# Kernel tuning notes

Measured on AMD Instinct MI355X. Metric: run time of the kernel, lower is better.

## Reference

```python
import jax, jax.numpy as jnp
import numpy as np

D_MODEL = 128; D_STATE = 16; D_CONV = 4; EXPAND = 2
D_INNER = EXPAND * D_MODEL          # 256
DT_RANK = (D_MODEL + 15) // 16      # 8 (ceil(d_model/16), Mamba default)
B, NF, H, W = 4, 32, 16, 16         # L = NF*H*W = 8192 tokens


def _layer_norm(x, w, b, eps=1e-5):
    m = x.mean(-1, keepdims=True)
    v = ((x - m) ** 2).mean(-1, keepdims=True)
    return (x - m) * jax.lax.rsqrt(v + eps) * w + b


def _causal_conv(x, w, b):
    # x: [B, L, D_INNER]; w: [D_INNER, 1, D_CONV] depthwise causal conv along L
    y = jax.lax.conv_general_dilated(
        jnp.swapaxes(x, 1, 2), w, (1,), [(D_CONV - 1, 0)],
        dimension_numbers=('NCH', 'OIH', 'NCH'), feature_group_count=D_INNER)
    return jnp.swapaxes(y + b[None, :, None], 1, 2)


def _mamba_dir(xi, z, conv_w, conv_b, xproj_w, dtproj_w, dtproj_b, A_log, Dskip):
    # One direction of the bidirectional Mamba block (selective scan).
    xc = jax.nn.silu(_causal_conv(xi, conv_w, conv_b))            # [B,L,Di]
    dbl = xc @ xproj_w.T                                          # [B,L,dt_rank+2n]
    dt_r, Bm, Cm = jnp.split(dbl, [DT_RANK, DT_RANK + D_STATE], axis=-1)
    dt = jax.nn.softplus(dt_r @ dtproj_w.T + dtproj_b)            # [B,L,Di]
    A = -jnp.exp(A_log)                                           # [Di,n]

    def step(h, inp):
        dt_t, B_t, C_t, x_t = inp                                 # [B,Di],[B,n],[B,n],[B,Di]
        h = jnp.exp(dt_t[:, :, None] * A) * h + (dt_t * x_t)[:, :, None] * B_t[:, None, :]
        return h, jnp.einsum('bdn,bn->bd', h, C_t)

    h0 = jnp.zeros((xi.shape[0], D_INNER, D_STATE), xi.dtype)
    xs = tuple(jnp.swapaxes(a, 0, 1) for a in (dt, Bm, Cm, xc))   # L-leading
    _, ys = jax.lax.scan(step, h0, xs)                            # [L,B,Di]
    y = jnp.swapaxes(ys, 0, 1) + xc * Dskip
    return y * jax.nn.silu(z)


def setup_inputs() -> dict:
    key = jax.random.key(0)
    ks = jax.random.split(key, 12)
    wrand = lambda k, shape: jax.random.normal(k, shape, jnp.float32) * 0.02
    # S4D-real init: A = [1..d_state] per channel
    A_init = jnp.log(jnp.tile(jnp.arange(1, D_STATE + 1, dtype=jnp.float32)[None, :], (D_INNER, 1)))
    dt_bias = jnp.full((D_INNER,), -4.6, jnp.float32)  # softplus^-1(~0.01)
    return {
        'x': jax.random.normal(ks[0], (B, D_MODEL, NF, H, W), jnp.float32),
        'ln1_w': jnp.ones((D_MODEL,), jnp.float32), 'ln1_b': jnp.zeros((D_MODEL,), jnp.float32),
        'ln2_w': jnp.ones((D_MODEL,), jnp.float32), 'ln2_b': jnp.zeros((D_MODEL,), jnp.float32),
        'in_proj_w': wrand(ks[1], (2 * D_INNER, D_MODEL)),
        'out_proj_w': wrand(ks[2], (D_MODEL, D_INNER)),
        'conv_w_f': wrand(ks[3], (D_INNER, 1, D_CONV)), 'conv_b_f': jnp.zeros((D_INNER,), jnp.float32),
        'xproj_w_f': wrand(ks[4], (DT_RANK + 2 * D_STATE, D_INNER)),
        'dtproj_w_f': wrand(ks[5], (D_INNER, DT_RANK)), 'dtproj_b_f': dt_bias,
        'A_log_f': A_init, 'D_f': jnp.ones((D_INNER,), jnp.float32),
        'conv_w_b': wrand(ks[6], (D_INNER, 1, D_CONV)), 'conv_b_b': jnp.zeros((D_INNER,), jnp.float32),
        'xproj_w_b': wrand(ks[7], (DT_RANK + 2 * D_STATE, D_INNER)),
        'dtproj_w_b': wrand(ks[8], (D_INNER, DT_RANK)), 'dtproj_b_b': dt_bias,
        'A_log_b': A_init, 'D_b': jnp.ones((D_INNER,), jnp.float32),
    }


def reference(x, ln1_w, ln1_b, ln2_w, ln2_b, in_proj_w, out_proj_w,
              conv_w_f, conv_b_f, xproj_w_f, dtproj_w_f, dtproj_b_f, A_log_f, D_f,
              conv_w_b, conv_b_b, xproj_w_b, dtproj_w_b, dtproj_b_b, A_log_b, D_b):
    b, d, nf, h, w = x.shape
    L = nf * h * w
    x_flat = jnp.swapaxes(x.reshape(b, d, L), 1, 2)               # [B,L,d_model]
    xn = _layer_norm(x_flat, ln1_w, ln1_b)
    xz = xn @ in_proj_w.T                                          # [B,L,2*Di]
    xi, z = jnp.split(xz, 2, axis=-1)
    y_f = _mamba_dir(xi, z, conv_w_f, conv_b_f, xproj_w_f, dtproj_w_f, dtproj_b_f, A_log_f, D_f)
    y_b = _mamba_dir(xi[:, ::-1], z[:, ::-1], conv_w_b, conv_b_b, xproj_w_b,
                     dtproj_w_b, dtproj_b_b, A_log_b, D_b)[:, ::-1]
    out = (y_f + y_b) @ out_proj_w.T                               # shared out_proj
    x_out = _layer_norm(x_flat + out, ln2_w, ln2_b)                # residual + norm2
    return jnp.swapaxes(x_out, 1, 2).reshape(b, d, nf, h, w)
```

## Files before the change

### kernel.cpp

```cpp
#include <hip/hip_runtime.h>

#define NB   4
#define LSEQ 8192
#define DM   128
#define DI   256
#define NS   16
#define RK   8
#define NCH  256
#define LC   32
#define MTOT (NB*LSEQ)
#define LOG2E 1.44269504088896340736f
#define LN2f  0.69314718055994530942f

#if __has_builtin(__builtin_amdgcn_exp2f)
__device__ __forceinline__ float fexp2(float x){ return __builtin_amdgcn_exp2f(x); }
#else
__device__ __forceinline__ float fexp2(float x){ return exp2f(x); }
#endif
#if __has_builtin(__builtin_amdgcn_logf)
__device__ __forceinline__ float flog2(float x){ return __builtin_amdgcn_logf(x); }
#else
__device__ __forceinline__ float flog2(float x){ return log2f(x); }
#endif
#if __has_builtin(__builtin_amdgcn_rcpf)
__device__ __forceinline__ float frcp(float x){ return __builtin_amdgcn_rcpf(x); }
#else
__device__ __forceinline__ float frcp(float x){ return 1.f/x; }
#endif
__device__ __forceinline__ float fexpn(float x){ return fexp2(x*LOG2E); }
__device__ __forceinline__ float fsilu(float x){ return x*frcp(1.f + fexpn(-x)); }
__device__ __forceinline__ float fsoftplus(float x){
  return fmaxf(x,0.f) + flog2(1.f + fexpn(-fabsf(x)))*LN2f;
}

__device__ __forceinline__ unsigned short f2bf(float v){
  unsigned int u = __float_as_uint(v);
  return (unsigned short)((u + 0x7FFFu + ((u >> 16) & 1u)) >> 16);
}
__device__ __forceinline__ float bf2f(unsigned short h){
  return __uint_as_float(((unsigned int)h) << 16);
}

typedef __attribute__((ext_vector_type(8))) short bf16x8;
typedef __attribute__((ext_vector_type(4))) float f32x4;
typedef __attribute__((ext_vector_type(2))) float f32x2;

#if __has_builtin(__builtin_elementwise_fma)
__device__ __forceinline__ f32x2 pkfma(f32x2 a, f32x2 b, f32x2 c){ return __builtin_elementwise_fma(a,b,c); }
#else
__device__ __forceinline__ f32x2 pkfma(f32x2 a, f32x2 b, f32x2 c){ return a*b + c; }
#endif

__global__ __launch_bounds__(256) void k_prep_w(
    const float* __restrict__ wip, unsigned short* __restrict__ wipbf,
    const float* __restrict__ xwf, const float* __restrict__ xwb, unsigned short* __restrict__ xwbf,
    const float* __restrict__ wop, unsigned short* __restrict__ wopbf)
{
  int i = blockIdx.x*256 + threadIdx.x;
  if (i < 65536) {
    wipbf[i] = f2bf(wip[i]);
  } else if (i < 90112) {
    int j = i - 65536;
    int dirw = j / 12288;
    int rem = j - dirw*12288;
    int row = rem >> 8, k = rem & 255;
    const float* src = dirw ? xwb : xwf;
    xwbf[j] = (row < 40) ? f2bf(src[row*256 + k]) : (unsigned short)0;
  } else {
    int j = i - 90112;
    wopbf[j] = f2bf(wop[j]);
  }
}

__global__ __launch_bounds__(256) void k_ln(
    const float* __restrict__ x, const float* __restrict__ ln1w, const float* __restrict__ ln1b,
    unsigned short* __restrict__ xnbf)
{
  __shared__ float a_s[DM][65];
  __shared__ float mS[64], rS[64];
  const int tid = threadIdx.x;
  const int m0 = blockIdx.x * 64;
  const int b = m0 >> 13, l0 = m0 & (LSEQ-1);
  const float* xb = x + b*DM*LSEQ;
#pragma unroll
  for (int i = 0; i < 32; ++i) {
    int idx = tid + i*256;
    int d = idx >> 6, l = idx & 63;
    a_s[d][l] = xb[d*LSEQ + l0 + l];
  }
  __syncthreads();
  {
    int p = tid & 3, l = tid >> 2;
    float s = 0.f, q = 0.f;
#pragma unroll
    for (int jj = 0; jj < 32; ++jj) {
      float v = a_s[p + 4*jj][l];
      s += v; q += v*v;
    }
    s += __shfl_xor(s,1); s += __shfl_xor(s,2);
    q += __shfl_xor(q,1); q += __shfl_xor(q,2);
    float m = s*(1.f/DM);
    float var = q*(1.f/DM) - m*m;
    if (p == 0) { mS[l] = m; rS[l] = rsqrtf(var + 1e-5f); }
  }
  __syncthreads();
#pragma unroll
  for (int i = 0; i < 32; ++i) {
    int idx = tid + i*256;
    int l = idx >> 7, d = idx & 127;
    float v = (a_s[d][l] - mS[l])*rS[l]*ln1w[d] + ln1b[d];
    xnbf[(m0+l)*DM + d] = f2bf(v);
  }
}

__global__ __launch_bounds__(256) void k_gemm_in(
    const unsigned short* __restrict__ xnbf, const unsigned short* __restrict__ wipbf,
    unsigned short* __restrict__ xib, unsigned short* __restrict__ zzb)
{
  __shared__ char lds[32768];
  const int tid = threadIdx.x;
  const int m0 = blockIdx.x * 64;
  const int n0 = blockIdx.y * 64;
  const unsigned short* srcs[2] = { xnbf + m0*DM, wipbf + n0*DM };
#pragma unroll
  for (int p = 0; p < 2; ++p) {
#pragma unroll
    for (int i = 0; i < 4; ++i) {
      int u = tid + i*256;
      int row = u >> 4, c = u & 15;
      int dstu = p*1024 + row*16 + (c ^ (row & 7));
      *(uint4*)(lds + dstu*16) = *(const uint4*)(srcs[p] + row*DM + c*8);
    }
  }
  __syncthreads();
  const int wid = tid >> 6, lane = tid & 63;
  const int m0w = (wid & 1)*32, n0w = (wid >> 1)*32;
  const int lr = lane & 15, kg = lane >> 4;
  bf16x8 af[2][4], bfv[2][4];
#pragma unroll
  for (int mi = 0; mi < 2; ++mi) {
    int row = m0w + mi*16 + lr;
#pragma unroll
    for (int kk = 0; kk < 4; ++kk) {
      int slot = (kk*4 + kg) ^ (row & 7);
      af[mi][kk] = *(const bf16x8*)(lds + row*256 + slot*16);
    }
  }
#pragma unroll
  for (int nj = 0; nj < 2; ++nj) {
    int row = n0w + nj*16 + lr;
#pragma unroll
    for (int kk = 0; kk < 4; ++kk) {
      int slot = (kk*4 + kg) ^ (row & 7);
      bfv[nj][kk] = *(const bf16x8*)(lds + 16384 + row*256 + slot*16);
    }
  }
  f32x4 acc[2][2];
#pragma unroll
  for (int mi = 0; mi < 2; ++mi)
#pragma unroll
    for (int nj = 0; nj < 2; ++nj) acc[mi][nj] = 0.f;
#pragma unroll
  for (int kk = 0; kk < 4; ++kk)
#pragma unroll
    for (int mi = 0; mi < 2; ++mi)
#pragma unroll
      for (int nj = 0; nj < 2; ++nj)
        acc[mi][nj] = __builtin_amdgcn_mfma_f32_16x16x32_bf16(af[mi][kk], bfv[nj][kk], acc[mi][nj], 0,0,0);
  if (n0 < 256) {
#pragma unroll
    for (int mi = 0; mi < 2; ++mi)
#pragma unroll
      for (int nj = 0; nj < 2; ++nj) {
        int n_g = n0 + n0w + nj*16 + lr;
#pragma unroll
        for (int r = 0; r < 4; ++r) {
          int m_g = m0 + m0w + mi*16 + kg*4 + r;
          xib[(size_t)m_g*DI + n_g] = f2bf(acc[mi][nj][r]);
        }
      }
  } else {
#pragma unroll
    for (int mi = 0; mi < 2; ++mi)
#pragma unroll
      for (int nj = 0; nj < 2; ++nj) {
        int n_g = (n0 - 256) + n0w + nj*16 + lr;
#pragma unroll
        for (int r = 0; r < 4; ++r) {
          int m_g = m0 + m0w + mi*16 + kg*4 + r;
          zzb[(size_t)m_g*DI + n_g] = f2bf(fsilu(acc[mi][nj][r]));
        }
      }
  }
}

__global__ __launch_bounds__(256) void k_conv_xproj(
  const unsigned short* __restrict__ xib,
  const float* __restrict__ cwf, const float* __restrict__ cbf,
  const float* __restrict__ cwb, const float* __restrict__ cbb,
  const unsigned short* __restrict__ xwbf,
  const float* __restrict__ dtwf, const float* __restrict__ dtbf,
  const float* __restrict__ dtwb, const float* __restrict__ dtbb,
  float* __restrict__ BC,
  uint4* __restrict__ xdt4)
{
  __shared__ char lds[57344];
  __shared__ float dtr_s[64][8];
  const int tid = threadIdx.x, bid = blockIdx.x;
  const int lt = bid & (LSEQ/64 - 1);
  const int b  = (bid >> 7) & 3;
  const int dir = bid >> 9;
  const int l0 = lt*64;
  const int db = dir*NB + b;
  const unsigned short* xwp = xwbf + dir*48*256;
#pragma unroll
  for (int i = 0; i < 6; ++i) {
    int u = tid + i*256;
    int row = u >> 5, s = u & 31;
    *(uint4*)(lds + 32768 + row*512 + ((s ^ (row & 7))<<4)) =
        *(const uint4*)(xwp + row*256 + s*8);
  }
  const float* cw  = dir ? cwb : cwf;
  const float* cbp = dir ? cbb : cbf;
  const int d = tid;
  const float w0 = cw[d*4+0], w1 = cw[d*4+1], w2 = cw[d*4+2], w3 = cw[d*4+3];
  const float bias = cbp[d];
  const int g0 = dir ? (LSEQ-1-l0) : l0;
  const int stp = dir ? -DI : DI;
  const unsigned short* xp = xib + (size_t)(b*LSEQ)*DI + d + (size_t)g0*DI;
  float h3 = 0.f, h2 = 0.f, h1 = 0.f;
  if (l0 >= 3) { h3 = bf2f(xp[-3*stp]); h2 = bf2f(xp[-2*stp]); h1 = bf2f(xp[-1*stp]); }
  float r0 = bf2f(xp[0]), r1 = bf2f(xp[stp]), r2 = bf2f(xp[2*stp]), r3 = bf2f(xp[3*stp]);
  for (int j = 0; j < 64; j += 4) {
    float v0 = r0, v1 = r1, v2 = r2, v3 = r3;
    if (j + 4 < 64) {
      const unsigned short* q = xp + (j+4)*stp;
      r0 = bf2f(q[0]); r1 = bf2f(q[stp]); r2 = bf2f(q[2*stp]); r3 = bf2f(q[3*stp]);
    }
#pragma unroll
    for (int u = 0; u < 4; ++u) {
      float vv = (u==0)?v0:(u==1)?v1:(u==2)?v2:v3;
      float a = bias + w0*h3 + w1*h2 + w2*h1 + w3*vv;
      int row = j + u;
      *(unsigned short*)(lds + row*512 + ((((d>>3) ^ (row&7))<<4) + ((d&7)<<1))) = f2bf(fsilu(a));
      h3 = h2; h2 = h1; h1 = vv;
    }
  }
  __syncthreads();
  const int wid = tid >> 6, lane = tid & 63;
  const int lr = lane & 15, kg = lane >> 4;
  const int arow = wid*16 + lr;
  f32x4 acc[3];
#pragma unroll
  for (int j = 0; j < 3; ++j) acc[j] = 0.f;
#pragma unroll
  for (int t = 0; t < 8; ++t) {
    bf16x8 afv = *(const bf16x8*)(lds + arow*512 + (((t*4+kg) ^ (arow&7))<<4));
#pragma unroll
    for (int j = 0; j < 3; ++j) {
      int wrow = j*16 + lr;
      bf16x8 bfr = *(const bf16x8*)(lds + 32768 + wrow*512 + (((t*4+kg) ^ (wrow&7))<<4));
      acc[j] = __builtin_amdgcn_mfma_f32_16x16x32_bf16(afv, bfr, acc[j], 0,0,0);
    }
  }
  const int base_l = (db*LSEQ + l0) + wid*16 + kg*4;
  const int rloc = wid*16 + kg*4;
#pragma unroll
  for (int j = 0; j < 3; ++j) {
    int col = j*16 + lr;
#pragma unroll
    for (int r = 0; r < 4; ++r) {
      float v = acc[j][r];
      if (col < 8)       dtr_s[rloc + r][col] = v;
      else if (col < 40) BC[(size_t)(base_l + r)*32 + (col - 8)] = v;
    }
  }
  __syncthreads();
  const float* dtw = dir ? dtwb : dtwf;
  const float* dtbp= dir ? dtbb : dtbf;
  float dwv[8];
  *(float4*)(dwv+0) = *(const float4*)&dtw[d*RK];
  *(float4*)(dwv+4) = *(const float4*)&dtw[d*RK+4];
  const float dtbv = dtbp[d];
  uint4* xdtp = xdt4 + (size_t)(db*(LSEQ/4) + (l0>>2))*DI + d;
  unsigned int a4[4];
  for (int row = 0; row < 64; ++row) {
    float sd = dtbv;
#pragma unroll
    for (int r = 0; r < RK; ++r) sd = fmaf(dtr_s[row][r], dwv[r], sd);
    unsigned short dtb = f2bf(fsoftplus(sd));
    unsigned short xcb = *(const unsigned short*)(lds + row*512 + ((((d>>3) ^ (row&7))<<4) + ((d&7)<<1)));
    a4[row & 3] = (unsigned int)xcb | ((unsigned int)dtb << 16);
    if ((row & 3) == 3)
      xdtp[(size_t)(row >> 2)*DI] = make_uint4(a4[0], a4[1], a4[2], a4[3]);
  }
}

__global__ __launch_bounds__(256) void k_scan_local(
  const uint4* __restrict__ xdt4, const float* __restrict__ BC,
  const float* __restrict__ alogf, const float* __restrict__ alogb,
  unsigned short* __restrict__ hloc, float* __restrict__ sumdt)
{
  const int tid = threadIdx.x, bid = blockIdx.x;
  const int c = bid & (NCH-1), b = (bid>>8)&3, dir = bid>>10;
  const int db = dir*NB + b;
  const int l0 = c*LC;
  const float* alog = dir ? alogb : alogf;
  const int d = tid;
  float A2[NS];
#pragma unroll
  for (int n = 0; n < NS; ++n) A2[n] = -fexpn(alog[d*NS+n]) * LOG2E;
  const float a20 = A2[0];
  bool pw = true;
#pragma unroll
  for (int n = 1; n < NS; ++n) pw = pw && (fabsf(A2[n] - (n+1)*a20) <= 1e-3f*fabsf(A2[n]));
  f32x2 h2[8];
#pragma unroll
  for (int k = 0; k < 8; ++k) h2[k] = 0.f;
  const uint4* xq = xdt4 + (size_t)(db*(LSEQ/4) + (l0>>2))*DI + d;
  const float* BCb = BC + (size_t)(db*LSEQ + l0)*32;
  uint4 X0 = xq[0];
  uint4 X1 = xq[DI];
  float sac = 0.f;
  for (int g = 0; g < 8; ++g) {
    uint4 cur = X0;
    X0 = X1;
    if (g + 2 < 8) X1 = xq[(size_t)(g+2)*DI];
    unsigned int us[4] = {cur.x, cur.y, cur.z, cur.w};
#pragma unroll
    for (int u = 0; u < 4; ++u) {
      unsigned int uu = us[u];
      float xc = __uint_as_float(uu << 16);
      float dt = __uint_as_float(uu & 0xffff0000u);
      sac += dt;
      float dx = dt*xc;
      const float4* bq = (const float4*)(BCb + (size_t)(g*4+u)*32);
      float bcl[16];
      *(float4*)(bcl+0)  = bq[0];
      *(float4*)(bcl+4)  = bq[1];
      *(float4*)(bcl+8)  = bq[2];
      *(float4*)(bcl+12) = bq[3];
      const f32x2* bb2 = (const f32x2*)bcl;
      f32x2 e2[8];
      if (pw) {
        float e1 = fexp2(a20*dt);
        float es = e1*e1;
        f32x2 esq = {es, es};
        e2[0] = (f32x2){e1, es};
#pragma unroll
        for (int k = 1; k < 8; ++k) e2[k] = e2[k-1]*esq;
      } else {
#pragma unroll
        for (int k = 0; k < 8; ++k)
          e2[k] = (f32x2){fexp2(A2[2*k]*dt), fexp2(A2[2*k+1]*dt)};
      }
      f32x2 dx2 = {dx, dx};
#pragma unroll
      for (int k = 0; k < 8; ++k) h2[k] = pkfma(h2[k], e2[k], bb2[k]*dx2);
    }
  }
  unsigned int hp8[8];
#pragma unroll
  for (int k = 0; k < 8; ++k)
    hp8[k] = (unsigned int)f2bf(h2[k].x) | ((unsigned int)f2bf(h2[k].y) << 16);
  unsigned short* dst = hloc + ((size_t)(db*NCH + c)*DI + d)*NS;
  *(uint4*)(dst)   = *(uint4*)(hp8);
  *(uint4*)(dst+8) = *(uint4*)(hp8+4);
  sumdt[(size_t)(db*NCH + c)*DI + d] = sac;
}

__global__ __launch_bounds__(64) void k_prefix(
  unsigned short* __restrict__ hloc, const float* __restrict__ sumdt,
  const float* __restrict__ alogf, const float* __restrict__ alogb)
{
  const int gid = blockIdx.x*64 + threadIdx.x;
  const int n = gid & 15;
  const int d = (gid >> 4) & 255;
  const int db = gid >> 12;
  const float* alog = (db >= NB) ? alogb : alogf;
  const float a2 = -fexpn(alog[d*NS+n]) * LOG2E;
  const int HS = DI*NS;
  unsigned short* hp = hloc + (size_t)db*NCH*HS + d*NS + n;
  const float* sp = sumdt + (size_t)db*NCH*DI + d;
  float hr = 0.f;
  float bl[16], bs[16];
#pragma unroll
  for (int j = 0; j < 16; ++j) { bl[j] = bf2f(hp[(size_t)j*HS]); bs[j] = sp[(size_t)j*DI]; }
  for (int blk = 0; blk < NCH/16; ++blk) {
    float nl[16], nsv[16];
    if (blk < NCH/16 - 1) {
#pragma unroll
      for (int j = 0; j < 16; ++j) {
        nl[j]  = bf2f(hp[(size_t)(blk*16+16+j)*HS]);
        nsv[j] = sp[(size_t)(blk*16+16+j)*DI];
      }
    }
#pragma unroll
    for (int j = 0; j < 16; ++j) {
      float hl = bl[j];
      hp[(size_t)(blk*16+j)*HS] = f2bf(hr);
      hr = fmaf(fexp2(a2*bs[j]), hr, hl);
    }
    if (blk < NCH/16 - 1) {
#pragma unroll
      for (int j = 0; j < 16; ++j) { bl[j] = nl[j]; bs[j] = nsv[j]; }
    }
  }
}

__global__ __launch_bounds__(256) void k_scan_out(
  const uint4* __restrict__ xdt4, const unsigned short* __restrict__ zzb,
  const float* __restrict__ BC,
  const unsigned short* __restrict__ hinb,
  const float* __restrict__ alogf, const float* __restrict__ alogb,
  const float* __restrict__ Dskf, const float* __restrict__ Dskb,
  unsigned short* __restrict__ s2bf)
{
  const int tid = threadIdx.x, bid = blockIdx.x;
  const int c = bid & (NCH-1), b = (bid>>8)&3, dir = bid>>10;
  const int db = dir*NB + b;
  const int l0 = c*LC;
  const float* alog = dir ? alogb : alogf;
  const int d = tid;
  const float Dd = (dir ? Dskb : Dskf)[d];
  float A2[NS];
#pragma unroll
  for (int n = 0; n < NS; ++n) A2[n] = -fexpn(alog[d*NS+n]) * LOG2E;
  const float a20 = A2[0];
  bool pw = true;
#pragma unroll
  for (int n = 1; n < NS; ++n) pw = pw && (fabsf(A2[n] - (n+1)*a20) <= 1e-3f*fabsf(A2[n]));
  f32x2 h2[8];
  {
    const unsigned short* hb = hinb + ((size_t)(db*NCH + c)*DI + d)*NS;
    uint4 p0 = *(const uint4*)(hb);
    uint4 p1 = *(const uint4*)(hb+8);
    unsigned int w[8] = {p0.x,p0.y,p0.z,p0.w,p1.x,p1.y,p1.z,p1.w};
#pragma unroll
    for (int k = 0; k < 8; ++k)
      h2[k] = (f32x2){__uint_as_float(w[k] << 16), __uint_as_float(w[k] & 0xffff0000u)};
  }
  const int g0 = dir ? (LSEQ-1-l0) : l0;
  const int stp = dir ? -DI : DI;
  const uint4* xq = xdt4 + (size_t)(db*(LSEQ/4) + (l0>>2))*DI + d;
  const float* BCb = BC + (size_t)(db*LSEQ + l0)*32;
  const unsigned short* zp = zzb + (size_t)(b*LSEQ + g0)*DI + d;
  unsigned short* sp = s2bf + (size_t)(db*LSEQ + l0)*DI + d;
  uint4 X0 = xq[0];
  uint4 X1 = xq[DI];
  unsigned short zA[4], zB[4];
#pragma unroll
  for (int k = 0; k < 4; ++k) { zA[k] = zp[k*stp]; zB[k] = zp[(4+k)*stp]; }
  for (int g = 0; g < 8; ++g) {
    uint4 cur = X0;
    X0 = X1;
    if (g + 2 < 8) X1 = xq[(size_t)(g+2)*DI];
    unsigned short zc[4];
#pragma unroll
    for (int k = 0; k < 4; ++k) zc[k] = zA[k];
#pragma unroll
    for (int k = 0; k < 4; ++k) zA[k] = zB[k];
    if (g + 2 < 8) {
#pragma unroll
      for (int k = 0; k < 4; ++k) zB[k] = zp[((g+2)*4+k)*stp];
    }
    unsigned int us[4] = {cur.x, cur.y, cur.z, cur.w};
#pragma unroll
    for (int u = 0; u < 4; ++u) {
      unsigned int uu = us[u];
      float xc = __uint_as_float(uu << 16);
      float dt = __uint_as_float(uu & 0xffff0000u);
      float dx = dt*xc;
      const float4* bq = (const float4*)(BCb + (size_t)(g*4+u)*32);
      float bcl[32];
      *(float4*)(bcl+0)  = bq[0];
      *(float4*)(bcl+4)  = bq[1];
      *(float4*)(bcl+8)  = bq[2];
      *(float4*)(bcl+12) = bq[3];
      *(float4*)(bcl+16) = bq[4];
      *(float4*)(bcl+20) = bq[5];
      *(float4*)(bcl+24) = bq[6];
      *(float4*)(bcl+28) = bq[7];
      const f32x2* bb2 = (const f32x2*)bcl;
      const f32x2* cc2 = (const f32x2*)(bcl + 16);
      f32x2 e2[8];
      if (pw) {
        float e1 = fexp2(a20*dt);
        float es = e1*e1;
        f32x2 esq = {es, es};
        e2[0] = (f32x2){e1, es};
#pragma unroll
        for (int k = 1; k < 8; ++k) e2[k] = e2[k-1]*esq;
      } else {
#pragma unroll
        for (int k = 0; k < 8; ++k)
          e2[k] = (f32x2){fexp2(A2[2*k]*dt), fexp2(A2[2*k+1]*dt)};
      }
      f32x2 dx2 = {dx, dx};
      f32x2 yv2 = {0.f, 0.f};
#pragma unroll
      for (int k = 0; k < 8; ++k) {
        h2[k] = pkfma(h2[k], e2[k], bb2[k]*dx2);
        yv2 = pkfma(h2[k], cc2[k], yv2);
      }
      float yv = yv2.x + yv2.y;
      yv = fmaf(xc, Dd, yv);
      sp[(size_t)(g*4+u)*DI] = f2bf(yv * bf2f(zc[u]));
    }
  }
}

__global__ __launch_bounds__(512) void k_out(
  const unsigned short* __restrict__ s2bf,
  const unsigned short* __restrict__ wopbf,
  const float* __restrict__ x, const float* __restrict__ ln2w, const float* __restrict__ ln2b,
  float* __restrict__ out)
{
  __shared__ char lds[65536];
  const int tid = threadIdx.x;
  const int m0 = blockIdx.x*64;
  const int b = m0 >> 13, l0 = m0 & (LSEQ-1);
  const unsigned short* sF = s2bf + (size_t)b*LSEQ*DI;
  const unsigned short* sB = s2bf + (size_t)(NB + b)*LSEQ*DI;
#pragma unroll
  for (int i = 0; i < 8; ++i) {
    int u = tid + i*512;
    int row = u >> 6, c = u & 63;
    int l = l0 + row;
    const unsigned short* src = (c < 32) ? (sF + (size_t)l*DI + c*8)
                                         : (sB + (size_t)(LSEQ-1-l)*DI + (c-32)*8);
    *(uint4*)(lds + row*1024 + ((c ^ (row & 7))<<4)) = *(const uint4*)src;
  }
  const int wid = tid >> 6;
  const int wr = wid >> 2, wc = wid & 3;
  const int lane = tid & 63, lr = lane & 15, kg = lane >> 4;
  bf16x8 wf[2][8];
#pragma unroll
  for (int nt = 0; nt < 2; ++nt) {
    int n = wc*32 + nt*16 + lr;
#pragma unroll
    for (int kt = 0; kt < 8; ++kt)
      wf[nt][kt] = *(const bf16x8*)(wopbf + n*DI + kt*32 + kg*8);
  }
  __syncthreads();
  f32x4 acc[2][2];
#pragma unroll
  for (int mt = 0; mt < 2; ++mt)
#pragma unroll
    for (int nt = 0; nt < 2; ++nt) acc[mt][nt] = 0.f;
#pragma unroll
  for (int kt2 = 0; kt2 < 16; ++kt2) {
#pragma unroll
    for (int mt = 0; mt < 2; ++mt) {
      int row = wr*32 + mt*16 + lr;
      int slot = (kt2*4 + kg) ^ (row & 7);
      bf16x8 af = *(const bf16x8*)(lds + row*1024 + (slot<<4));
#pragma unroll
      for (int nt = 0; nt < 2; ++nt)
        acc[mt][nt] = __builtin_amdgcn_mfma_f32_16x16x32_bf16(af, wf[nt][kt2 & 7], acc[mt][nt], 0,0,0);
    }
  }
  __syncthreads();
  float* smem = (float*)lds;
  const int RP = 133;
  float* mS = smem + 64*RP;
  float* rS = mS + 64;
  const float* xb = x + b*DM*LSEQ + l0;
#pragma unroll
  for (int mt = 0; mt < 2; ++mt) {
    int mbase = wr*32 + mt*16 + kg*4;
#pragma unroll
    for (int nt = 0; nt < 2; ++nt) {
      int n = wc*32 + nt*16 + lr;
      float4 rx = *(const float4*)&xb[n*LSEQ + mbase];
      smem[(mbase+0)*RP + n] = acc[mt][nt][0] + rx.x;
      smem[(mbase+1)*RP + n] = acc[mt][nt][1] + rx.y;
      smem[(mbase+2)*RP + n] = acc[mt][nt][2] + rx.z;
      smem[(mbase+3)*RP + n] = acc[mt][nt][3] + rx.w;
    }
  }
  __syncthreads();
  {
    int row = tid >> 3, p = tid & 7;
    float s = 0.f, q = 0.f;
#pragma unroll
    for (int jj = 0; jj < 16; ++jj) {
      float v = smem[row*RP + p*16 + jj];
      s += v; q += v*v;
    }
    s += __shfl_xor(s,1); s += __shfl_xor(s,2); s += __shfl_xor(s,4);
    q += __shfl_xor(q,1); q += __shfl_xor(q,2); q += __shfl_xor(q,4);
    if (p == 0) {
      float m = s*(1.f/DM);
      float var = q*(1.f/DM) - m*m;
      mS[row] = m; rS[row] = rsqrtf(var + 1e-5f);
    }
  }
  __syncthreads();
  float* ob = out + b*DM*LSEQ + l0;
#pragma unroll
  for (int i = 0; i < 16; ++i) {
    int idx = tid + i*512;
    int col = idx >> 6, l = idx & 63;
    float v = (smem[l*RP + col] - mS[l])*rS[l]*ln2w[col] + ln2b[col];
    ob[col*LSEQ + l] = v;
  }
}

extern "C" void kernel_launch(void* const* d_in, const int* in_sizes, int n_in,
                              void* d_out, int out_size, void* d_ws, size_t ws_size,
                              hipStream_t stream)
{
  (void)in_sizes; (void)n_in; (void)out_size; (void)ws_size;
  const float* x     = (const float*)d_in[0];
  const float* ln1w  = (const float*)d_in[1];
  const float* ln1b  = (const float*)d_in[2];
  const float* ln2w  = (const float*)d_in[3];
  const float* ln2b  = (const float*)d_in[4];
  const float* wip   = (const float*)d_in[5];
  const float* wop   = (const float*)d_in[6];
  const float* cwf   = (const float*)d_in[7];
  const float* cbf   = (const float*)d_in[8];
  const float* xwf   = (const float*)d_in[9];
  const float* dtwf  = (const float*)d_in[10];
  const float* dtbf  = (const float*)d_in[11];
  const float* alogf = (const float*)d_in[12];
  const float* Dskf  = (const float*)d_in[13];
  const float* cwb   = (const float*)d_in[14];
  const float* cbb   = (const float*)d_in[15];
  const float* xwb   = (const float*)d_in[16];
  const float* dtwb  = (const float*)d_in[17];
  const float* dtbb  = (const float*)d_in[18];
  const float* alogb = (const float*)d_in[19];
  const float* Dskb  = (const float*)d_in[20];

  float* ws    = (float*)d_ws;
  float* xibF  = ws;
  float* zzbF  = xibF  + 4194304;
  float* BC    = zzbF  + 4194304;
  float* s2F   = BC    + 2097184;
  float* xdtF  = s2F   + 8388608;
  float* hlocF = xdtF  + 16777216;
  float* sumdt = hlocF + 4194304;
  float* xwbfF = sumdt + 524288;
  float* wopbfF= xwbfF + 12288;
  float* out   = (float*)d_out;
  unsigned short* xnbf  = (unsigned short*)s2F;
  unsigned short* wipbf = (unsigned short*)(s2F + 2097152);
  unsigned short* s2bf  = (unsigned short*)s2F;
  unsigned short* xib   = (unsigned short*)xibF;
  unsigned short* zzb   = (unsigned short*)zzbF;
  uint4*          xdt4  = (uint4*)xdtF;
  unsigned short* hloc  = (unsigned short*)hlocF;
  unsigned short* xwbf  = (unsigned short*)xwbfF;
  unsigned short* wopbf = (unsigned short*)wopbfF;

  k_prep_w<<<480, 256, 0, stream>>>(wip, wipbf, xwf, xwb, xwbf, wop, wopbf);
  k_ln<<<512, 256, 0, stream>>>(x, ln1w, ln1b, xnbf);
  k_gemm_in<<<dim3(512,8), 256, 0, stream>>>(xnbf, wipbf, xib, zzb);
  k_conv_xproj<<<1024, 256, 0, stream>>>(xib, cwf,cbf,cwb,cbb, xwbf,
                                         dtwf,dtbf,dtwb,dtbb, BC, xdt4);
  k_scan_local<<<2048, 256, 0, stream>>>(xdt4, BC, alogf, alogb, hloc, sumdt);
  k_prefix<<<512, 64, 0, stream>>>(hloc, sumdt, alogf, alogb);
  k_scan_out<<<2048, 256, 0, stream>>>(xdt4, zzb, BC, hloc,
                                       alogf, alogb, Dskf, Dskb, s2bf);
  k_out<<<512, 512, 0, stream>>>(s2bf, wopbf, x, ln2w, ln2b, out);
}
```

Baseline: 168.2 us.

## Compute local scan output in first pass and apply carry-in correction in second

The first chunked-scan pass now also produces the chunk-local output y (with the D skip term) and the running cumulative dt, writing both in place over the xc/dt buffer as bf16 pairs. The second pass no longer reruns the recurrence. It adds the carried-in state's contribution, C·(exp(A·cumdt)·h_in), to the stored local output and then multiplies by silu(z). This removes the B loads and the state-update FMAs from the second pass, at the cost of extra C loads and output writes in the first pass. Storing cumulative dt and partial y in bf16 may add precision error.

```diff
diff --git a/kernel.cpp b/kernel.cpp
--- a/kernel.cpp
+++ b/kernel.cpp
@@ -296,9 +296,11 @@
   }
 }
 
-__global__ __launch_bounds__(256) void k_scan_local(
-  const uint4* __restrict__ xdt4, const float* __restrict__ BC,
+__global__ __launch_bounds__(256) void k_scan_fwd(
+  uint4* xy,
+  const float* __restrict__ BC,
   const float* __restrict__ alogf, const float* __restrict__ alogb,
+  const float* __restrict__ Dskf, const float* __restrict__ Dskb,
   unsigned short* __restrict__ hloc, float* __restrict__ sumdt)
 {
   const int tid = threadIdx.x, bid = blockIdx.x;
@@ -307,6 +309,7 @@
   const int l0 = c*LC;
   const float* alog = dir ? alogb : alogf;
   const int d = tid;
+  const float Dd = (dir ? Dskb : Dskf)[d];
   float A2[NS];
 #pragma unroll
   for (int n = 0; n < NS; ++n) A2[n] = -fexpn(alog[d*NS+n]) * LOG2E;
@@ -317,16 +320,15 @@
   f32x2 h2[8];
 #pragma unroll
   for (int k = 0; k < 8; ++k) h2[k] = 0.f;
-  const uint4* xq = xdt4 + (size_t)(db*(LSEQ/4) + (l0>>2))*DI + d;
+  uint4* xq = xy + (size_t)(db*(LSEQ/4) + (l0>>2))*DI + d;
   const float* BCb = BC + (size_t)(db*LSEQ + l0)*32;
-  uint4 X0 = xq[0];
-  uint4 X1 = xq[DI];
+  uint4 Xn = xq[0];
   float sac = 0.f;
   for (int g = 0; g < 8; ++g) {
-    uint4 cur = X0;
-    X0 = X1;
-    if (g + 2 < 8) X1 = xq[(size_t)(g+2)*DI];
+    uint4 cur = Xn;
+    if (g + 1 < 8) Xn = xq[(size_t)(g+1)*DI];
     unsigned int us[4] = {cur.x, cur.y, cur.z, cur.w};
+    unsigned int outp[4];
 #pragma unroll
     for (int u = 0; u < 4; ++u) {
       unsigned int uu = us[u];
@@ -335,12 +337,13 @@
       sac += dt;
       float dx = dt*xc;
       const float4* bq = (const float4*)(BCb + (size_t)(g*4+u)*32);
-      float bcl[16];
-      *(float4*)(bcl+0)  = bq[0];
-      *(float4*)(bcl+4)  = bq[1];
-      *(float4*)(bcl+8)  = bq[2];
-      *(float4*)(bcl+12) = bq[3];
+      float bcl[32];
+      *(float4*)(bcl+0)  = bq[0];  *(float4*)(bcl+4)  = bq[1];
+      *(float4*)(bcl+8)  = bq[2];  *(float4*)(bcl+12) = bq[3];
+      *(float4*)(bcl+16) = bq[4];  *(float4*)(bcl+20) = bq[5];
+      *(float4*)(bcl+24) = bq[6];  *(float4*)(bcl+28) = bq[7];
       const f32x2* bb2 = (const f32x2*)bcl;
+      const f32x2* cc2 = (const f32x2*)(bcl + 16);
       f32x2 e2[8];
       if (pw) {
         float e1 = fexp2(a20*dt);
@@ -355,9 +358,16 @@
           e2[k] = (f32x2){fexp2(A2[2*k]*dt), fexp2(A2[2*k+1]*dt)};
       }
       f32x2 dx2 = {dx, dx};
-#pragma unroll
-      for (int k = 0; k < 8; ++k) h2[k] = pkfma(h2[k], e2[k], bb2[k]*dx2);
-    }
+      f32x2 yv2 = {0.f, 0.f};
+#pragma unroll
+      for (int k = 0; k < 8; ++k) {
+        h2[k] = pkfma(h2[k], e2[k], bb2[k]*dx2);
+        yv2 = pkfma(h2[k], cc2[k], yv2);
+      }
+      float yv = fmaf(xc, Dd, yv2.x + yv2.y);
+      outp[u] = (unsigned int)f2bf(yv) | ((unsigned int)f2bf(sac) << 16);
+    }
+    xq[(size_t)g*DI] = make_uint4(outp[0], outp[1], outp[2], outp[3]);
   }
   unsigned int hp8[8];
 #pragma unroll
@@ -408,12 +418,11 @@
   }
 }
 
-__global__ __launch_bounds__(256) void k_scan_out(
-  const uint4* __restrict__ xdt4, const unsigned short* __restrict__ zzb,
+__global__ __launch_bounds__(256) void k_correct(
+  const uint4* __restrict__ ycd, const unsigned short* __restrict__ zzb,
   const float* __restrict__ BC,
   const unsigned short* __restrict__ hinb,
   const float* __restrict__ alogf, const float* __restrict__ alogb,
-  const float* __restrict__ Dskf, const float* __restrict__ Dskb,
   unsigned short* __restrict__ s2bf)
 {
   const int tid = threadIdx.x, bid = blockIdx.x;
@@ -422,7 +431,6 @@
   const int l0 = c*LC;
   const float* alog = dir ? alogb : alogf;
   const int d = tid;
-  const float Dd = (dir ? Dskb : Dskf)[d];
   float A2[NS];
 #pragma unroll
   for (int n = 0; n < NS; ++n) A2[n] = -fexpn(alog[d*NS+n]) * LOG2E;
@@ -430,7 +438,7 @@
   bool pw = true;
 #pragma unroll
   for (int n = 1; n < NS; ++n) pw = pw && (fabsf(A2[n] - (n+1)*a20) <= 1e-3f*fabsf(A2[n]));
-  f32x2 h2[8];
+  f32x2 g2[8];
   {
     const unsigned short* hb = hinb + ((size_t)(db*NCH + c)*DI + d)*NS;
     uint4 p0 = *(const uint4*)(hb);
@@ -438,54 +446,32 @@
     unsigned int w[8] = {p0.x,p0.y,p0.z,p0.w,p1.x,p1.y,p1.z,p1.w};
 #pragma unroll
     for (int k = 0; k < 8; ++k)
-      h2[k] = (f32x2){__uint_as_float(w[k] << 16), __uint_as_float(w[k] & 0xffff0000u)};
+      g2[k] = (f32x2){__uint_as_float(w[k] << 16), __uint_as_float(w[k] & 0xffff0000u)};
   }
   const int g0 = dir ? (LSEQ-1-l0) : l0;
   const int stp = dir ? -DI : DI;
-  const uint4* xq = xdt4 + (size_t)(db*(LSEQ/4) + (l0>>2))*DI + d;
+  const uint4* yq = ycd + (size_t)(db*(LSEQ/4) + (l0>>2))*DI + d;
   const float* BCb = BC + (size_t)(db*LSEQ + l0)*32;
   const unsigned short* zp = zzb + (size_t)(b*LSEQ + g0)*DI + d;
   unsigned short* sp = s2bf + (size_t)(db*LSEQ + l0)*DI + d;
-  uint4 X0 = xq[0];
-  uint4 X1 = xq[DI];
-  unsigned short zA[4], zB[4];
-#pragma unroll
-  for (int k = 0; k < 4; ++k) { zA[k] = zp[k*stp]; zB[k] = zp[(4+k)*stp]; }
+  uint4 Xn = yq[0];
   for (int g = 0; g < 8; ++g) {
-    uint4 cur = X0;
-    X0 = X1;
-    if (g + 2 < 8) X1 = xq[(size_t)(g+2)*DI];
-    unsigned short zc[4];
-#pragma unroll
-    for (int k = 0; k < 4; ++k) zc[k] = zA[k];
-#pragma unroll
-    for (int k = 0; k < 4; ++k) zA[k] = zB[k];
-    if (g + 2 < 8) {
-#pragma unroll
-      for (int k = 0; k < 4; ++k) zB[k] = zp[((g+2)*4+k)*stp];
-    }
+    uint4 cur = Xn;
+    if (g + 1 < 8) Xn = yq[(size_t)(g+1)*DI];
     unsigned int us[4] = {cur.x, cur.y, cur.z, cur.w};
 #pragma unroll
     for (int u = 0; u < 4; ++u) {
       unsigned int uu = us[u];
-      float xc = __uint_as_float(uu << 16);
-      float dt = __uint_as_float(uu & 0xffff0000u);
-      float dx = dt*xc;
-      const float4* bq = (const float4*)(BCb + (size_t)(g*4+u)*32);
-      float bcl[32];
-      *(float4*)(bcl+0)  = bq[0];
-      *(float4*)(bcl+4)  = bq[1];
-      *(float4*)(bcl+8)  = bq[2];
-      *(float4*)(bcl+12) = bq[3];
-      *(float4*)(bcl+16) = bq[4];
-      *(float4*)(bcl+20) = bq[5];
-      *(float4*)(bcl+24) = bq[6];
-      *(float4*)(bcl+28) = bq[7];
-      const f32x2* bb2 = (const f32x2*)bcl;
-      const f32x2* cc2 = (const f32x2*)(bcl + 16);
+      float yl = __uint_as_float(uu << 16);
+      float cd = __uint_as_float(uu & 0xffff0000u);
+      const float4* cq = (const float4*)(BCb + (size_t)(g*4+u)*32 + 16);
+      float ccl[16];
+      *(float4*)(ccl+0)  = cq[0];  *(float4*)(ccl+4)  = cq[1];
+      *(float4*)(ccl+8)  = cq[2];  *(float4*)(ccl+12) = cq[3];
+      const f32x2* cc2 = (const f32x2*)ccl;
       f32x2 e2[8];
       if (pw) {
-        float e1 = fexp2(a20*dt);
+        float e1 = fexp2(a20*cd);
         float es = e1*e1;
         f32x2 esq = {es, es};
         e2[0] = (f32x2){e1, es};
@@ -494,18 +480,14 @@
       } else {
 #pragma unroll
         for (int k = 0; k < 8; ++k)
-          e2[k] = (f32x2){fexp2(A2[2*k]*dt), fexp2(A2[2*k+1]*dt)};
+          e2[k] = (f32x2){fexp2(A2[2*k]*cd), fexp2(A2[2*k+1]*cd)};
       }
-      f32x2 dx2 = {dx, dx};
       f32x2 yv2 = {0.f, 0.f};
 #pragma unroll
-      for (int k = 0; k < 8; ++k) {
-        h2[k] = pkfma(h2[k], e2[k], bb2[k]*dx2);
-        yv2 = pkfma(h2[k], cc2[k], yv2);
-      }
-      float yv = yv2.x + yv2.y;
-      yv = fmaf(xc, Dd, yv);
-      sp[(size_t)(g*4+u)*DI] = f2bf(yv * bf2f(zc[u]));
+      for (int k = 0; k < 8; ++k)
+        yv2 = pkfma(g2[k]*e2[k], cc2[k], yv2);
+      float s = (yl + yv2.x + yv2.y) * bf2f(zp[(g*4+u)*stp]);
+      sp[(size_t)(g*4+u)*DI] = f2bf(s);
     }
   }
 }
@@ -660,9 +642,10 @@
   k_gemm_in<<<dim3(512,8), 256, 0, stream>>>(xnbf, wipbf, xib, zzb);
   k_conv_xproj<<<1024, 256, 0, stream>>>(xib, cwf,cbf,cwb,cbb, xwbf,
                                          dtwf,dtbf,dtwb,dtbb, BC, xdt4);
-  k_scan_local<<<2048, 256, 0, stream>>>(xdt4, BC, alogf, alogb, hloc, sumdt);
+  k_scan_fwd<<<2048, 256, 0, stream>>>(xdt4, BC, alogf, alogb, Dskf, Dskb,
+                                       hloc, sumdt);
   k_prefix<<<512, 64, 0, stream>>>(hloc, sumdt, alogf, alogb);
-  k_scan_out<<<2048, 256, 0, stream>>>(xdt4, zzb, BC, hloc,
-                                       alogf, alogb, Dskf, Dskb, s2bf);
+  k_correct<<<2048, 256, 0, stream>>>(xdt4, zzb, BC, hloc,
+                                      alogf, alogb, s2bf);
   k_out<<<512, 512, 0, stream>>>(s2bf, wopbf, x, ln2w, ln2b, out);
 }
```

After: 181.5 us. +7.9%, slower.
